# Kernel tuning notes

Measured on AMD Instinct MI355X. Metric: run time of the kernel, lower is better.

The kernel has to match this reference:

```python
import jax, jax.numpy as jnp
import numpy as np

EPS = 1e-5  # torch InstanceNorm1d default eps


def _instance_norm(x, gamma, beta):
    # per-sample, per-channel stats over the length dim; biased variance (torch semantics)
    mu = jnp.mean(x, axis=-1, keepdims=True)
    var = jnp.var(x, axis=-1, keepdims=True)
    return (x - mu) / jnp.sqrt(var + EPS) * gamma[None, :, None] + beta[None, :, None]


def _forward(x_ft, gamma, beta):
    # x_ft: complex [B, C, N]
    N = x_ft.shape[-1]
    x = jnp.real(jnp.fft.ifft(x_ft, norm='forward'))  # [B, C, N] real
    # The torch loop runs res = base_res .. N, each iteration overwriting the
    # low/high frequency bands of x_out in-place. The final iteration
    # (res == N) writes EVERY entry of x_out (the two band slices cover all
    # N//2+1 rfft bins), so the module's output -- and its gradients, since
    # overwritten writes carry zero cotangent -- equal the res == N
    # computation alone. resample_1d(x, N) copies the full spectrum and is a
    # spectral identity, so x_res == x.
    xr = _instance_norm(x, gamma, beta)
    xr = jax.nn.gelu(xr, approximate=False)  # exact GELU, matches torch nn.GELU
    # Faithful to the source: inside the loop torch.fft.rfft2 is used, i.e. a
    # 2D transform over the last two dims (channel, length).
    x_out = jnp.fft.rfft2(xr, norm='forward')  # complex [B, C, N//2 + 1]
    out = jnp.fft.fft(jnp.fft.irfft(x_out, n=N, norm='forward'), norm='forward')
    return out  # complex [B, C, N]


def setup_inputs() -> dict:
    key = jax.random.key(0)
    k1, k2 = jax.random.split(key)
    B, C, N = 16, 128, 8192
    return {
        'x_ft_real': jax.random.normal(k1, (B, C, N), dtype=jnp.float32),
        'x_ft_imag': jax.random.normal(k2, (B, C, N), dtype=jnp.float32),
        'gamma': jnp.ones((C,), dtype=jnp.float32),
        'beta': jnp.zeros((C,), dtype=jnp.float32),
    }


def reference(x_ft_real, x_ft_imag, gamma, beta):
    out = _forward(jax.lax.complex(x_ft_real, x_ft_imag), gamma, beta)
    # return real/imag parts as separate float arrays (harness-friendly)
    return (jnp.real(out), jnp.imag(out))
```

## Files before the change

kernel.cpp:

```cpp
#include <hip/hip_runtime.h>
#include <math.h>

static constexpr int kN = 8192;
static constexpr int kC = 128;
static constexpr int kB = 16;
static constexpr float kScale = 0.5f / 1048576.0f;
static constexpr double kTwoPi = 6.28318530717958647692;

#define C8  0.70710678118654752f
#define CP8 0.92387953251128676f
#define SP8 0.38268343236508977f

typedef float v2f __attribute__((ext_vector_type(2)));

__device__ __forceinline__ v2f mk2(float x, float y){ v2f r; r.x=x; r.y=y; return r; }
__device__ __forceinline__ v2f imul(v2f a){ return mk2(-a.y, a.x); }
__device__ __forceinline__ v2f mimul(v2f a){ return mk2(a.y, -a.x); }
__device__ __forceinline__ v2f cconj(v2f a){ return mk2(a.x, -a.y); }
__device__ __forceinline__ v2f cmul(v2f a, v2f b){
    return mk2(a.x*b.x - a.y*b.y, a.x*b.y + a.y*b.x);
}

__device__ __forceinline__ int swz(int n){ return n ^ ((n>>4)&15); }

__device__ __forceinline__ v2f W2048(const v2f* T, int m){
    v2f tt = T[m & 1023];
    return (m & 1024) ? imul(tt) : tt;
}

#define REV(k) ((((k)&3)<<2)|((k)>>2))

template<int SGN>
__device__ __forceinline__ void dft4(v2f&a, v2f&b, v2f&c, v2f&d){
    v2f t0=a+c, t1=a-c, t2=b+d, t3=b-d;
    v2f j3 = (SGN>0) ? imul(t3) : mimul(t3);
    a = t0+t2; b = t1+j3; c = t0-t2; d = t1-j3;
}

template<int SGN>
__device__ __forceinline__ void dft16(v2f* v){
    dft4<SGN>(v[0], v[4], v[8],  v[12]);
    dft4<SGN>(v[1], v[5], v[9],  v[13]);
    dft4<SGN>(v[2], v[6], v[10], v[14]);
    dft4<SGN>(v[3], v[7], v[11], v[15]);
    const float sg = (SGN>0)? 1.f : -1.f;
    const v2f W1 = mk2(CP8,  sg*SP8);
    const v2f W2 = mk2(C8,   sg*C8);
    const v2f W3 = mk2(SP8,  sg*CP8);
    const v2f W6 = mk2(-C8,  sg*C8);
    const v2f W9 = mk2(-CP8, -sg*SP8);
    v[5]  = cmul(v[5],  W1);
    v[9]  = cmul(v[9],  W2);
    v[13] = cmul(v[13], W3);
    v[6]  = cmul(v[6],  W2);
    v[10] = (SGN>0)? imul(v[10]) : mimul(v[10]);
    v[14] = cmul(v[14], W6);
    v[7]  = cmul(v[7],  W3);
    v[11] = cmul(v[11], W6);
    v[15] = cmul(v[15], W9);
    dft4<SGN>(v[0],  v[1],  v[2],  v[3]);
    dft4<SGN>(v[4],  v[5],  v[6],  v[7]);
    dft4<SGN>(v[8],  v[9],  v[10], v[11]);
    dft4<SGN>(v[12], v[13], v[14], v[15]);
}

__device__ __forceinline__ void twid_dif(v2f* v, v2f w1){
    v2f w2=cmul(w1,w1), w3=cmul(w2,w1), w4=cmul(w2,w2);
    v2f w5=cmul(w2,w3), w6=cmul(w3,w3), w7=cmul(w3,w4), w8=cmul(w4,w4);
    v2f w9=cmul(w4,w5), w10=cmul(w5,w5), w11=cmul(w5,w6), w12=cmul(w6,w6);
    v2f w13=cmul(w6,w7), w14=cmul(w7,w7), w15=cmul(w7,w8);
    v[4] =cmul(v[4], w1);  v[8] =cmul(v[8], w2);  v[12]=cmul(v[12],w3);
    v[1] =cmul(v[1], w4);  v[5] =cmul(v[5], w5);  v[9] =cmul(v[9], w6);
    v[13]=cmul(v[13],w7);  v[2] =cmul(v[2], w8);  v[6] =cmul(v[6], w9);
    v[10]=cmul(v[10],w10); v[14]=cmul(v[14],w11); v[3] =cmul(v[3], w12);
    v[7] =cmul(v[7], w13); v[11]=cmul(v[11],w14); v[15]=cmul(v[15],w15);
}

__device__ __forceinline__ void twid_dit(v2f* v, v2f w1){
    v2f w2=cmul(w1,w1), w3=cmul(w2,w1), w4=cmul(w2,w2);
    v2f w5=cmul(w2,w3), w6=cmul(w3,w3), w7=cmul(w3,w4), w8=cmul(w4,w4);
    v2f w9=cmul(w4,w5), w10=cmul(w5,w5), w11=cmul(w5,w6), w12=cmul(w6,w6);
    v2f w13=cmul(w6,w7), w14=cmul(w7,w7), w15=cmul(w7,w8);
    v[1] =cmul(v[1], w1);  v[2] =cmul(v[2], w2);  v[3] =cmul(v[3], w3);
    v[4] =cmul(v[4], w4);  v[5] =cmul(v[5], w5);  v[6] =cmul(v[6], w6);
    v[7] =cmul(v[7], w7);  v[8] =cmul(v[8], w8);  v[9] =cmul(v[9], w9);
    v[10]=cmul(v[10],w10); v[11]=cmul(v[11],w11); v[12]=cmul(v[12],w12);
    v[13]=cmul(v[13],w13); v[14]=cmul(v[14],w14); v[15]=cmul(v[15],w15);
}

__device__ __forceinline__ v2f gelu2(v2f v){
    v2f z = v * (0.7978845608028654f + 0.0356774081363001f * v * v);
    float e0 = __builtin_amdgcn_exp2f(-2.8853900817779268f * z.x);
    float e1 = __builtin_amdgcn_exp2f(-2.8853900817779268f * z.y);
    return mk2(v.x / (1.0f + e0), v.y / (1.0f + e1));
}

__global__ __launch_bounds__(256, 4) void k1_row(
    const float* __restrict__ xr, const float* __restrict__ xi,
    const float* __restrict__ gamma, const float* __restrict__ beta,
    float* __restrict__ outR, float* __restrict__ outI)
{
    __shared__ v2f buf[4096];
    __shared__ v2f T[1024];

    const int p   = threadIdx.x;
    const int row = blockIdx.x;
    const int ch  = row & (kC-1);

    for (int i = p; i < 1024; i += 256) {
        float s, c;
        sincosf((float)(kTwoPi/4096.0 * (double)i), &s, &c);
        T[i] = mk2(c, s);
    }
    __syncthreads();

    const v2f E = mk2(0.9999997058628822f, 7.669903187427045e-4f);
    const int i0 = ((p>>4)<<8) + (p&15);
    const v2f wB = T[(p&15)<<4];

    v2f v[16];

    const float* rR = xr + (size_t)row * kN;
    const float* rI = xi + (size_t)row * kN;

    #pragma unroll
    for (int j = 0; j < 16; ++j) {
        int k   = p + (j<<8);
        int km  = (kN - k) & (kN-1);
        int km2 = 4096 - k;
        v2f w = W2048(T, k>>1);
        if (p & 1) w = cmul(w, E);
        v2f Hk  = mk2(rR[k]+rR[km],       rI[k]-rI[km]);
        v2f Hk2 = mk2(rR[k+4096]+rR[km2], rI[k+4096]-rI[km2]);
        v2f S = Hk + Hk2, D = Hk - Hk2;
        v2f P = cmul(D, w);
        v[j] = S + imul(P);
    }
    dft16<1>(v);
    twid_dif(v, T[p]);
    #pragma unroll
    for (int m = 0; m < 16; ++m) buf[swz(p + (m<<8))] = v[REV(m)];
    __syncthreads();

    #pragma unroll
    for (int j = 0; j < 16; ++j) v[j] = buf[swz(i0 + (j<<4))];
    dft16<1>(v);
    twid_dif(v, wB);
    #pragma unroll
    for (int m = 0; m < 16; ++m) buf[swz(i0 + (m<<4))] = v[REV(m)];
    __syncthreads();

    #pragma unroll
    for (int j = 0; j < 16; ++j) v[j] = buf[swz((p<<4) + j)];
    dft16<1>(v);

    float ps = 0.f, pq = 0.f;
    #pragma unroll
    for (int j = 0; j < 16; ++j) {
        ps += v[j].x + v[j].y;
        pq += v[j].x*v[j].x + v[j].y*v[j].y;
    }
    #pragma unroll
    for (int off = 32; off >= 1; off >>= 1) {
        ps += __shfl_down(ps, off);
        pq += __shfl_down(pq, off);
    }
    if ((p & 63) == 0) buf[swz(p<<4)] = mk2(ps, pq);
    __syncthreads();
    float sum = 0.f, sq = 0.f;
    #pragma unroll
    for (int w = 0; w < 4; ++w) {
        v2f pr = buf[swz((w<<6)<<4)];
        sum += pr.x; sq += pr.y;
    }
    __syncthreads();
    float mean = sum * (1.0f/8192.0f);
    float var  = sq  * (1.0f/8192.0f) - mean*mean;
    float gg = gamma[ch] * rsqrtf(var + 1e-5f);
    float bb = beta[ch] - mean * gg;
    #pragma unroll
    for (int j = 0; j < 16; ++j) v[j] = gelu2(v[j] * gg + bb);

    {
        v2f u[16];
        #pragma unroll
        for (int j = 0; j < 16; ++j) u[j] = v[REV(j)];
        dft16<-1>(u);
        #pragma unroll
        for (int m = 0; m < 16; ++m) buf[swz((p<<4) + m)] = u[REV(m)];
    }
    __syncthreads();

    #pragma unroll
    for (int j = 0; j < 16; ++j) v[j] = buf[swz(i0 + (j<<4))];
    twid_dit(v, cconj(wB));
    dft16<-1>(v);
    #pragma unroll
    for (int m = 0; m < 16; ++m) buf[swz(i0 + (m<<4))] = v[REV(m)];
    __syncthreads();

    #pragma unroll
    for (int j = 0; j < 16; ++j) v[j] = buf[swz(p + (j<<8))];
    twid_dit(v, cconj(T[p]));
    dft16<-1>(v);
    float* oR = outR + (size_t)row * kN;
    float* oI = outI + (size_t)row * kN;
    #pragma unroll
    for (int m = 0; m < 16; ++m) {
        int k = p + (m<<8);
        oR[k] = v[REV(m)].x;
        oI[k] = v[REV(m)].y;
    }
}

__global__ __launch_bounds__(256, 4) void k2_col(float* __restrict__ outR,
                                                 float* __restrict__ outI)
{
    __shared__ v2f tile[kC][32];
    __shared__ v2f tw[64];

    const int tid  = threadIdx.x;
    const int b    = blockIdx.y;
    const int k0   = blockIdx.x << 4;
    const int jj   = tid & 15;
    const int cw   = tid >> 4;
    const int colA = k0 + jj;
    const bool valid = (colA <= 2048);
    const int colB = (4096 - colA) & 4095;

    if (tid < 64) {
        float s, c;
        sincosf((float)(kTwoPi/128.0 * (double)tid), &s, &c);
        tw[tid] = mk2(c, -s);
    }

    float ws, wc;
    sincosf((float)(-kTwoPi/8192.0 * (double)colA), &ws, &wc);

    float* baseR = outR + (size_t)b * kC * kN;
    float* baseI = outI + (size_t)b * kC * kN;

    for (int c = cw; c < kC; c += 16) {
        v2f YA = mk2(0.f,0.f), YB = mk2(0.f,0.f);
        if (valid) {
            size_t offA = (size_t)c * kN + colA;
            size_t offB = (size_t)c * kN + colB;
            float Zx  = baseR[offA], Zy  = baseI[offA];
            float Zmx = baseR[offB], Zmy = baseI[offB];
            float Sx = Zx + Zmx, Sy = Zy - Zmy;
            float Dx = Zx - Zmx, Dy = Zy + Zmy;
            float Px = Dx*wc - Dy*ws, Py = Dx*ws + Dy*wc;
            YA = mk2(Sx + Py,  Sy - Px);
            YB = mk2(Sx - Py, -Sy - Px);
        }
        tile[c][jj]      = YA;
        tile[c][jj + 16] = YB;
    }
    __syncthreads();

    const int kc = tid & 31;
    const int wq = tid >> 5;
    for (int st = 7; st >= 1; --st) {
        const int h = 1 << (st-1);
        #pragma unroll
        for (int s = 0; s < 8; ++s) {
            int q   = wq + (s<<3);
            int pos = q & (h-1);
            int g0  = ((q >> (st-1)) << st) + pos;
            int g1  = g0 + h;
            v2f a = tile[g0][kc], bb = tile[g1][kc];
            v2f w = tw[pos << (7-st)];
            tile[g0][kc] = a + bb;
            tile[g1][kc] = cmul(a - bb, w);
        }
        __syncthreads();
    }

    const int cA = (kc < 16) ? (k0 + kc) : (k0 + kc - 16);
    const int kk = (kc < 16) ? cA : (4096 - cA);
    if (cA <= 2048) {
        for (int pch = wq; pch < kC; pch += 8) {
            int f = (int)(__brev((unsigned)pch) >> 25);
            v2f vv = tile[pch][kc] * kScale;
            size_t off = (size_t)f * kN + kk;
            if (kk == 0 || kk == 4096) {
                baseR[off] = vv.x; baseI[off] = 0.f;
            } else {
                baseR[off] = vv.x; baseI[off] = vv.y;
                size_t offm = (size_t)f * kN + (kN - kk);
                baseR[offm] = vv.x; baseI[offm] = -vv.y;
            }
        }
    }
}

extern "C" void kernel_launch(void* const* d_in, const int* in_sizes, int n_in,
                              void* d_out, int out_size, void* d_ws, size_t ws_size,
                              hipStream_t stream)
{
    const float* xr    = (const float*)d_in[0];
    const float* xi    = (const float*)d_in[1];
    const float* gamma = (const float*)d_in[2];
    const float* beta  = (const float*)d_in[3];

    float* outR = (float*)d_out;
    float* outI = outR + (size_t)kB * kC * kN;

    k1_row<<<kB * kC, 256, 0, stream>>>(xr, xi, gamma, beta, outR, outI);
    k2_col<<<dim3(129, kB), 256, 0, stream>>>(outR, outI);
}
```

Measured before the change: 129.4 us.

## Compute twiddles with fast sincos and move rfft post-processing into row kernel

Drops the shared-memory twiddle table and its setup sync in the row kernel. Every twiddle is now computed directly with __sincosf instead of table lookups and power chains. The real-FFT split/post-processing step moves from the column kernel into the end of the row kernel through an extra LDS pass, so the column kernel only loads already-split bins. Occupancy hint for the row kernel rises to 5 blocks. This removes the table init and the paired gathers in k2, but adds many transcendental evaluations per thread and may lose some twiddle accuracy.

```diff
diff --git a/kernel.cpp b/kernel.cpp
--- a/kernel.cpp
+++ b/kernel.cpp
@@ -10,6 +10,7 @@
 #define C8  0.70710678118654752f
 #define CP8 0.92387953251128676f
 #define SP8 0.38268343236508977f
+#define TWO_PI_F 6.2831853071795864769f
 
 typedef float v2f __attribute__((ext_vector_type(2)));
 
@@ -21,12 +22,13 @@
     return mk2(a.x*b.x - a.y*b.y, a.x*b.y + a.y*b.x);
 }
 
+__device__ __forceinline__ v2f wrev(float rev){
+    float s, c;
+    __sincosf(rev * TWO_PI_F, &s, &c);
+    return mk2(c, s);
+}
+
 __device__ __forceinline__ int swz(int n){ return n ^ ((n>>4)&15); }
-
-__device__ __forceinline__ v2f W2048(const v2f* T, int m){
-    v2f tt = T[m & 1023];
-    return (m & 1024) ? imul(tt) : tt;
-}
 
 #define REV(k) ((((k)&3)<<2)|((k)>>2))
 
@@ -64,28 +66,23 @@
     dft4<SGN>(v[12], v[13], v[14], v[15]);
 }
 
-__device__ __forceinline__ void twid_dif(v2f* v, v2f w1){
-    v2f w2=cmul(w1,w1), w3=cmul(w2,w1), w4=cmul(w2,w2);
-    v2f w5=cmul(w2,w3), w6=cmul(w3,w3), w7=cmul(w3,w4), w8=cmul(w4,w4);
-    v2f w9=cmul(w4,w5), w10=cmul(w5,w5), w11=cmul(w5,w6), w12=cmul(w6,w6);
-    v2f w13=cmul(w6,w7), w14=cmul(w7,w7), w15=cmul(w7,w8);
-    v[4] =cmul(v[4], w1);  v[8] =cmul(v[8], w2);  v[12]=cmul(v[12],w3);
-    v[1] =cmul(v[1], w4);  v[5] =cmul(v[5], w5);  v[9] =cmul(v[9], w6);
-    v[13]=cmul(v[13],w7);  v[2] =cmul(v[2], w8);  v[6] =cmul(v[6], w9);
-    v[10]=cmul(v[10],w10); v[14]=cmul(v[14],w11); v[3] =cmul(v[3], w12);
-    v[7] =cmul(v[7], w13); v[11]=cmul(v[11],w14); v[15]=cmul(v[15],w15);
-}
-
-__device__ __forceinline__ void twid_dit(v2f* v, v2f w1){
-    v2f w2=cmul(w1,w1), w3=cmul(w2,w1), w4=cmul(w2,w2);
-    v2f w5=cmul(w2,w3), w6=cmul(w3,w3), w7=cmul(w3,w4), w8=cmul(w4,w4);
-    v2f w9=cmul(w4,w5), w10=cmul(w5,w5), w11=cmul(w5,w6), w12=cmul(w6,w6);
-    v2f w13=cmul(w6,w7), w14=cmul(w7,w7), w15=cmul(w7,w8);
-    v[1] =cmul(v[1], w1);  v[2] =cmul(v[2], w2);  v[3] =cmul(v[3], w3);
-    v[4] =cmul(v[4], w4);  v[5] =cmul(v[5], w5);  v[6] =cmul(v[6], w6);
-    v[7] =cmul(v[7], w7);  v[8] =cmul(v[8], w8);  v[9] =cmul(v[9], w9);
-    v[10]=cmul(v[10],w10); v[11]=cmul(v[11],w11); v[12]=cmul(v[12],w12);
-    v[13]=cmul(v[13],w13); v[14]=cmul(v[14],w14); v[15]=cmul(v[15],w15);
+template<int SGN>
+__device__ __forceinline__ void twid_dif_sc(v2f* v, int q, float inv){
+    #pragma unroll
+    for (int m = 1; m < 16; ++m) {
+        v2f w = wrev((float)(q*m) * inv);
+        if (SGN < 0) w = cconj(w);
+        v[REV(m)] = cmul(v[REV(m)], w);
+    }
+}
+template<int SGN>
+__device__ __forceinline__ void twid_dit_sc(v2f* v, int q, float inv){
+    #pragma unroll
+    for (int m = 1; m < 16; ++m) {
+        v2f w = wrev((float)(q*m) * inv);
+        if (SGN < 0) w = cconj(w);
+        v[m] = cmul(v[m], w);
+    }
 }
 
 __device__ __forceinline__ v2f gelu2(v2f v){
@@ -95,28 +92,19 @@
     return mk2(v.x / (1.0f + e0), v.y / (1.0f + e1));
 }
 
-__global__ __launch_bounds__(256, 4) void k1_row(
+__global__ __launch_bounds__(256, 5) void k1_row(
     const float* __restrict__ xr, const float* __restrict__ xi,
     const float* __restrict__ gamma, const float* __restrict__ beta,
     float* __restrict__ outR, float* __restrict__ outI)
 {
     __shared__ v2f buf[4096];
-    __shared__ v2f T[1024];
 
     const int p   = threadIdx.x;
     const int row = blockIdx.x;
     const int ch  = row & (kC-1);
 
-    for (int i = p; i < 1024; i += 256) {
-        float s, c;
-        sincosf((float)(kTwoPi/4096.0 * (double)i), &s, &c);
-        T[i] = mk2(c, s);
-    }
-    __syncthreads();
-
-    const v2f E = mk2(0.9999997058628822f, 7.669903187427045e-4f);
     const int i0 = ((p>>4)<<8) + (p&15);
-    const v2f wB = T[(p&15)<<4];
+    const int qB = p & 15;
 
     v2f v[16];
 
@@ -128,8 +116,7 @@
         int k   = p + (j<<8);
         int km  = (kN - k) & (kN-1);
         int km2 = 4096 - k;
-        v2f w = W2048(T, k>>1);
-        if (p & 1) w = cmul(w, E);
+        v2f w = wrev((float)k * (1.0f/8192.0f));
         v2f Hk  = mk2(rR[k]+rR[km],       rI[k]-rI[km]);
         v2f Hk2 = mk2(rR[k+4096]+rR[km2], rI[k+4096]-rI[km2]);
         v2f S = Hk + Hk2, D = Hk - Hk2;
@@ -137,7 +124,7 @@
         v[j] = S + imul(P);
     }
     dft16<1>(v);
-    twid_dif(v, T[p]);
+    twid_dif_sc<1>(v, p, 1.0f/4096.0f);
     #pragma unroll
     for (int m = 0; m < 16; ++m) buf[swz(p + (m<<8))] = v[REV(m)];
     __syncthreads();
@@ -145,7 +132,7 @@
     #pragma unroll
     for (int j = 0; j < 16; ++j) v[j] = buf[swz(i0 + (j<<4))];
     dft16<1>(v);
-    twid_dif(v, wB);
+    twid_dif_sc<1>(v, qB, 1.0f/256.0f);
     #pragma unroll
     for (int m = 0; m < 16; ++m) buf[swz(i0 + (m<<4))] = v[REV(m)];
     __syncthreads();
@@ -193,7 +180,7 @@
 
     #pragma unroll
     for (int j = 0; j < 16; ++j) v[j] = buf[swz(i0 + (j<<4))];
-    twid_dit(v, cconj(wB));
+    twid_dit_sc<-1>(v, qB, 1.0f/256.0f);
     dft16<-1>(v);
     #pragma unroll
     for (int m = 0; m < 16; ++m) buf[swz(i0 + (m<<4))] = v[REV(m)];
@@ -201,94 +188,84 @@
 
     #pragma unroll
     for (int j = 0; j < 16; ++j) v[j] = buf[swz(p + (j<<8))];
-    twid_dit(v, cconj(T[p]));
+    twid_dit_sc<-1>(v, p, 1.0f/4096.0f);
     dft16<-1>(v);
+    #pragma unroll
+    for (int m = 0; m < 16; ++m) buf[swz(p + (m<<8))] = v[REV(m)];
+    __syncthreads();
+
     float* oR = outR + (size_t)row * kN;
     float* oI = outI + (size_t)row * kN;
     #pragma unroll
     for (int m = 0; m < 16; ++m) {
         int k = p + (m<<8);
-        oR[k] = v[REV(m)].x;
-        oI[k] = v[REV(m)].y;
-    }
-}
-
-__global__ __launch_bounds__(256, 4) void k2_col(float* __restrict__ outR,
-                                                 float* __restrict__ outI)
+        v2f Z  = v[REV(m)];
+        v2f Zm = buf[swz((4096 - k) & 4095)];
+        v2f w = cconj(wrev((float)k * (1.0f/8192.0f)));
+        v2f S = mk2(Z.x+Zm.x, Z.y-Zm.y);
+        v2f D = mk2(Z.x-Zm.x, Z.y+Zm.y);
+        v2f Y = S + mimul(cmul(D, w));
+        oR[k] = Y.x;  oI[k] = Y.y;
+    }
+    if (p == 0) {
+        oR[4096] = 2.0f*(v[0].x - v[0].y);
+        oI[4096] = 0.f;
+    }
+}
+
+__global__ __launch_bounds__(256,4) void k2_col(float* __restrict__ outR,
+                                                float* __restrict__ outI)
 {
     __shared__ v2f tile[kC][32];
     __shared__ v2f tw[64];
 
-    const int tid  = threadIdx.x;
-    const int b    = blockIdx.y;
-    const int k0   = blockIdx.x << 4;
-    const int jj   = tid & 15;
-    const int cw   = tid >> 4;
-    const int colA = k0 + jj;
-    const bool valid = (colA <= 2048);
-    const int colB = (4096 - colA) & 4095;
+    const int tid = threadIdx.x;
+    const int k   = tid & 31;
+    const int g   = tid >> 5;
+    const int b   = blockIdx.y;
+    const int kk  = (blockIdx.x << 5) + k;
+    const bool valid = (kk <= 4096);
 
     if (tid < 64) {
         float s, c;
         sincosf((float)(kTwoPi/128.0 * (double)tid), &s, &c);
         tw[tid] = mk2(c, -s);
     }
-
-    float ws, wc;
-    sincosf((float)(-kTwoPi/8192.0 * (double)colA), &ws, &wc);
-
     float* baseR = outR + (size_t)b * kC * kN;
     float* baseI = outI + (size_t)b * kC * kN;
-
-    for (int c = cw; c < kC; c += 16) {
-        v2f YA = mk2(0.f,0.f), YB = mk2(0.f,0.f);
-        if (valid) {
-            size_t offA = (size_t)c * kN + colA;
-            size_t offB = (size_t)c * kN + colB;
-            float Zx  = baseR[offA], Zy  = baseI[offA];
-            float Zmx = baseR[offB], Zmy = baseI[offB];
-            float Sx = Zx + Zmx, Sy = Zy - Zmy;
-            float Dx = Zx - Zmx, Dy = Zy + Zmy;
-            float Px = Dx*wc - Dy*ws, Py = Dx*ws + Dy*wc;
-            YA = mk2(Sx + Py,  Sy - Px);
-            YB = mk2(Sx - Py, -Sy - Px);
-        }
-        tile[c][jj]      = YA;
-        tile[c][jj + 16] = YB;
-    }
-    __syncthreads();
-
-    const int kc = tid & 31;
-    const int wq = tid >> 5;
+    for (int c = g; c < kC; c += 8) {
+        size_t off = (size_t)c * kN + kk;
+        tile[c][k] = valid ? mk2(baseR[off], baseI[off]) : mk2(0.f, 0.f);
+    }
+    __syncthreads();
+
     for (int st = 7; st >= 1; --st) {
         const int h = 1 << (st-1);
         #pragma unroll
         for (int s = 0; s < 8; ++s) {
-            int q   = wq + (s<<3);
+            int q   = g + (s<<3);
             int pos = q & (h-1);
-            int g0  = ((q >> (st-1)) << st) + pos;
-            int g1  = g0 + h;
-            v2f a = tile[g0][kc], bb = tile[g1][kc];
+            int i0  = ((q >> (st-1)) << st) + pos;
+            int i1  = i0 + h;
+            v2f a = tile[i0][k], bb = tile[i1][k];
             v2f w = tw[pos << (7-st)];
-            tile[g0][kc] = a + bb;
-            tile[g1][kc] = cmul(a - bb, w);
+            tile[i0][k] = a + bb;
+            tile[i1][k] = cmul(a - bb, w);
         }
         __syncthreads();
     }
 
-    const int cA = (kc < 16) ? (k0 + kc) : (k0 + kc - 16);
-    const int kk = (kc < 16) ? cA : (4096 - cA);
-    if (cA <= 2048) {
-        for (int pch = wq; pch < kC; pch += 8) {
-            int f = (int)(__brev((unsigned)pch) >> 25);
-            v2f vv = tile[pch][kc] * kScale;
+    if (valid) {
+        for (int p = g; p < kC; p += 8) {
+            int f = (int)(__brev((unsigned)p) >> 25);
+            v2f v = tile[p][k] * kScale;
             size_t off = (size_t)f * kN + kk;
             if (kk == 0 || kk == 4096) {
-                baseR[off] = vv.x; baseI[off] = 0.f;
+                baseR[off] = v.x; baseI[off] = 0.f;
             } else {
-                baseR[off] = vv.x; baseI[off] = vv.y;
+                baseR[off] = v.x; baseI[off] = v.y;
                 size_t offm = (size_t)f * kN + (kN - kk);
-                baseR[offm] = vv.x; baseI[offm] = -vv.y;
+                baseR[offm] = v.x; baseI[offm] = -v.y;
             }
         }
     }
```

Result: slower. 305.2 us (+135.9%).

## Widen column kernel to 32 columns per block with two-pass B-half FFT

Applied to the files above, without the earlier changes.

The column kernel now handles 32 consecutive columns per block instead of 16, so global loads and stores cover wider contiguous segments. The second-half (mirrored) values are kept in registers and run through a second 128-point column FFT pass after the first half is written out, which halves the grid. Twiddle generation switches from sincosf to the hardware sin/cos builtins, and launch bounds drop to 2 waves per SIMD. The trade-offs are more registers, twice the barriers per block, and slightly lower twiddle accuracy.

```diff
diff --git a/kernel.cpp b/kernel.cpp
--- a/kernel.cpp
+++ b/kernel.cpp
@@ -75,7 +75,6 @@
     v[10]=cmul(v[10],w10); v[14]=cmul(v[14],w11); v[3] =cmul(v[3], w12);
     v[7] =cmul(v[7], w13); v[11]=cmul(v[11],w14); v[15]=cmul(v[15],w15);
 }
-
 __device__ __forceinline__ void twid_dit(v2f* v, v2f w1){
     v2f w2=cmul(w1,w1), w3=cmul(w2,w1), w4=cmul(w2,w2);
     v2f w5=cmul(w2,w3), w6=cmul(w3,w3), w7=cmul(w3,w4), w8=cmul(w4,w4);
@@ -213,35 +212,36 @@
     }
 }
 
-__global__ __launch_bounds__(256, 4) void k2_col(float* __restrict__ outR,
+__global__ __launch_bounds__(256, 2) void k2_col(float* __restrict__ outR,
                                                  float* __restrict__ outI)
 {
     __shared__ v2f tile[kC][32];
     __shared__ v2f tw[64];
 
     const int tid  = threadIdx.x;
+    const int j    = tid & 31;
+    const int g    = tid >> 5;
     const int b    = blockIdx.y;
-    const int k0   = blockIdx.x << 4;
-    const int jj   = tid & 15;
-    const int cw   = tid >> 4;
-    const int colA = k0 + jj;
+    const int k0   = blockIdx.x << 5;
+    const int colA = k0 + j;
     const bool valid = (colA <= 2048);
     const int colB = (4096 - colA) & 4095;
 
     if (tid < 64) {
-        float s, c;
-        sincosf((float)(kTwoPi/128.0 * (double)tid), &s, &c);
-        tw[tid] = mk2(c, -s);
-    }
-
-    float ws, wc;
-    sincosf((float)(-kTwoPi/8192.0 * (double)colA), &ws, &wc);
+        tw[tid] = mk2(__builtin_amdgcn_cosf((float)tid * (1.0f/128.0f)),
+                      -__builtin_amdgcn_sinf((float)tid * (1.0f/128.0f)));
+    }
+    const float wc =  __builtin_amdgcn_cosf((float)colA * (1.0f/8192.0f));
+    const float ws = -__builtin_amdgcn_sinf((float)colA * (1.0f/8192.0f));
 
     float* baseR = outR + (size_t)b * kC * kN;
     float* baseI = outI + (size_t)b * kC * kN;
 
-    for (int c = cw; c < kC; c += 16) {
-        v2f YA = mk2(0.f,0.f), YB = mk2(0.f,0.f);
+    v2f yb[16];
+    #pragma unroll
+    for (int ci = 0; ci < 16; ++ci) {
+        const int c = g + (ci << 3);
+        v2f YA = mk2(0.f, 0.f), YB = mk2(0.f, 0.f);
         if (valid) {
             size_t offA = (size_t)c * kN + colA;
             size_t offB = (size_t)c * kN + colB;
@@ -253,41 +253,75 @@
             YA = mk2(Sx + Py,  Sy - Px);
             YB = mk2(Sx - Py, -Sy - Px);
         }
-        tile[c][jj]      = YA;
-        tile[c][jj + 16] = YB;
-    }
-    __syncthreads();
-
-    const int kc = tid & 31;
-    const int wq = tid >> 5;
+        tile[c][j] = YA;
+        yb[ci] = YB;
+    }
+    __syncthreads();
+
     for (int st = 7; st >= 1; --st) {
         const int h = 1 << (st-1);
         #pragma unroll
         for (int s = 0; s < 8; ++s) {
-            int q   = wq + (s<<3);
+            int q   = g + (s<<3);
             int pos = q & (h-1);
-            int g0  = ((q >> (st-1)) << st) + pos;
-            int g1  = g0 + h;
-            v2f a = tile[g0][kc], bb = tile[g1][kc];
+            int i0  = ((q >> (st-1)) << st) + pos;
+            int i1  = i0 + h;
+            v2f a = tile[i0][j], bb = tile[i1][j];
             v2f w = tw[pos << (7-st)];
-            tile[g0][kc] = a + bb;
-            tile[g1][kc] = cmul(a - bb, w);
+            tile[i0][j] = a + bb;
+            tile[i1][j] = cmul(a - bb, w);
         }
         __syncthreads();
     }
-
-    const int cA = (kc < 16) ? (k0 + kc) : (k0 + kc - 16);
-    const int kk = (kc < 16) ? cA : (4096 - cA);
-    if (cA <= 2048) {
-        for (int pch = wq; pch < kC; pch += 8) {
-            int f = (int)(__brev((unsigned)pch) >> 25);
-            v2f vv = tile[pch][kc] * kScale;
-            size_t off = (size_t)f * kN + kk;
-            if (kk == 0 || kk == 4096) {
+    if (valid) {
+        for (int p = g; p < kC; p += 8) {
+            int f = (int)(__brev((unsigned)p) >> 25);
+            v2f vv = tile[p][j] * kScale;
+            size_t off = (size_t)f * kN + colA;
+            if (colA == 0) {
                 baseR[off] = vv.x; baseI[off] = 0.f;
             } else {
                 baseR[off] = vv.x; baseI[off] = vv.y;
-                size_t offm = (size_t)f * kN + (kN - kk);
+                size_t offm = (size_t)f * kN + (kN - colA);
+                baseR[offm] = vv.x; baseI[offm] = -vv.y;
+            }
+        }
+    }
+    __syncthreads();
+
+    #pragma unroll
+    for (int ci = 0; ci < 16; ++ci) {
+        const int c = g + (ci << 3);
+        tile[c][j] = yb[ci];
+    }
+    __syncthreads();
+
+    for (int st = 7; st >= 1; --st) {
+        const int h = 1 << (st-1);
+        #pragma unroll
+        for (int s = 0; s < 8; ++s) {
+            int q   = g + (s<<3);
+            int pos = q & (h-1);
+            int i0  = ((q >> (st-1)) << st) + pos;
+            int i1  = i0 + h;
+            v2f a = tile[i0][j], bb = tile[i1][j];
+            v2f w = tw[pos << (7-st)];
+            tile[i0][j] = a + bb;
+            tile[i1][j] = cmul(a - bb, w);
+        }
+        __syncthreads();
+    }
+    if (valid) {
+        const int kkB = 4096 - colA;
+        for (int p = g; p < kC; p += 8) {
+            int f = (int)(__brev((unsigned)p) >> 25);
+            v2f vv = tile[p][j] * kScale;
+            size_t off = (size_t)f * kN + kkB;
+            if (kkB == 4096) {
+                baseR[off] = vv.x; baseI[off] = 0.f;
+            } else {
+                baseR[off] = vv.x; baseI[off] = vv.y;
+                size_t offm = (size_t)f * kN + (kN - kkB);
                 baseR[offm] = vv.x; baseI[offm] = -vv.y;
             }
         }
@@ -307,5 +341,5 @@
     float* outI = outR + (size_t)kB * kC * kN;
 
     k1_row<<<kB * kC, 256, 0, stream>>>(xr, xi, gamma, beta, outR, outI);
-    k2_col<<<dim3(129, kB), 256, 0, stream>>>(outR, outI);
-}
+    k2_col<<<dim3(65, kB), 256, 0, stream>>>(outR, outI);
+}
```

Result: faster. 115.3 us (-10.9%).
